# Optimization experiments

Measured on AMD Instinct MI355X. Metric: run time of the kernel, lower is better.

## Reference

```python
import jax, jax.numpy as jnp
import numpy as np

L = 8        # num_layers
B = 4        # batch
S = 1024     # seq_len
D = 1024     # hidden_size
H = 16       # num_heads
FC = 4096    # fc_size
NEG = -1e9   # additive causal-mask value (matches torch code's -1000000000.0)


def setup_inputs() -> dict:
    key = jax.random.key(0)
    ks = jax.random.split(key, 12)
    std = 0.02
    inputs = jax.random.normal(ks[0], (B, S, D), jnp.float32)
    # per-layer stacked parameters; torch Linear y = x W^T + b, here stored as [in, out]
    Wq = jax.random.normal(ks[1], (L, D, D), jnp.float32) * std
    Wk = jax.random.normal(ks[2], (L, D, D), jnp.float32) * std
    Wv = jax.random.normal(ks[3], (L, D, D), jnp.float32) * std
    Wo = jax.random.normal(ks[4], (L, D, D), jnp.float32) * std
    W1 = jax.random.normal(ks[5], (L, D, FC), jnp.float32) * std
    W2 = jax.random.normal(ks[6], (L, FC, D), jnp.float32) * std
    bq = jnp.zeros((L, D), jnp.float32)
    bk = jnp.zeros((L, D), jnp.float32)
    bv = jnp.zeros((L, D), jnp.float32)
    bo = jnp.zeros((L, D), jnp.float32)
    b1 = jnp.zeros((L, FC), jnp.float32)
    b2 = jnp.zeros((L, D), jnp.float32)
    ln_g = jnp.ones((D,), jnp.float32)   # single LayerNorm shared across all sites
    ln_b = jnp.zeros((D,), jnp.float32)
    scale = jnp.asarray(0.1, jnp.float32)  # re-zero residual scale (init 0 in torch; 0.1 for non-degenerate test)
    return dict(inputs=inputs, Wq=Wq, bq=bq, Wk=Wk, bk=bk, Wv=Wv, bv=bv,
                Wo=Wo, bo=bo, W1=W1, b1=b1, W2=W2, b2=b2,
                ln_g=ln_g, ln_b=ln_b, scale=scale)


def reference(inputs, Wq, bq, Wk, bk, Wv, bv, Wo, bo, W1, b1, W2, b2, ln_g, ln_b, scale):
    Bz, Sl, Dm = inputs.shape
    nL = Wq.shape[0]
    dh = Dm // H
    inv_sqrt_dh = 1.0 / np.sqrt(dh).astype(np.float32)

    def layer_norm(x):  # shared gamma/beta, eps matches torch default 1e-5
        mu = jnp.mean(x, axis=-1, keepdims=True)
        var = jnp.var(x, axis=-1, keepdims=True)
        return (x - mu) * jax.lax.rsqrt(var + 1e-5) * ln_g + ln_b

    # causal additive bias [S, S], broadcasts over [B, H, S, S]
    bias = jnp.triu(jnp.full((Sl, Sl), NEG, inputs.dtype), k=1)

    x = inputs
    for i in range(nL):
        # --- masked self-attention block ---
        r = layer_norm(x)
        q = (r @ Wq[i] + bq[i]).reshape(Bz, Sl, H, dh)
        k = (r @ Wk[i] + bk[i]).reshape(Bz, Sl, H, dh)
        v = (r @ Wv[i] + bv[i]).reshape(Bz, Sl, H, dh)
        logits = jnp.einsum('bqhd,bkhd->bhqk', q, k) * inv_sqrt_dh + bias
        attn = jax.nn.softmax(logits, axis=-1)
        vals = jnp.einsum('bhqk,bkhd->bqhd', attn, v).reshape(Bz, Sl, Dm)
        r = vals @ Wo[i] + bo[i]
        x = x + scale * r  # re-zero residual (dropout is identity at inference)
        # --- FFN block ---
        r = layer_norm(x)
        r = jax.nn.gelu(r @ W1[i] + b1[i], approximate=False) @ W2[i] + b2[i]
        x = x + scale * r
    return layer_norm(x)
```

## Files before the change

kernel.cpp:

```cpp
#include <hip/hip_runtime.h>


typedef __bf16 bf16x8 __attribute__((ext_vector_type(8)));
typedef float  f32x4  __attribute__((ext_vector_type(4)));
typedef unsigned int u32x4 __attribute__((ext_vector_type(4)));

#define DEV static __device__ __forceinline__

DEV unsigned short f2bf(float x) {
  unsigned u = __builtin_bit_cast(unsigned int, x);
  u += 0x7fffu + ((u >> 16) & 1u);
  return (unsigned short)(u >> 16);
}

DEV unsigned int pack2bf(float lo, float hi) {
  return (unsigned int)f2bf(lo) | ((unsigned int)f2bf(hi) << 16);
}

DEV f32x4 mfma16(bf16x8 a, bf16x8 b, f32x4 c) {
  return __builtin_amdgcn_mfma_f32_16x16x32_bf16(a, b, c, 0, 0, 0);
}

DEV bf16x8 ldb8(const unsigned short* p) {
  return *reinterpret_cast<const bf16x8*>(p);
}

DEV void gload_lds16(const unsigned short* g, unsigned short* l) {
  __builtin_amdgcn_global_load_lds(
      (const __attribute__((address_space(1))) void*)g,
      (__attribute__((address_space(3))) void*)l, 16, 0, 0);
}

__global__ void transpose_cvt(const float* __restrict__ src,
                              unsigned short* __restrict__ dst,
                              int srcStride, int dstStride) {
  __shared__ float tile[32][33];
  const int t  = threadIdx.x;
  const int r  = t >> 3;
  const int c4 = (t & 7) << 2;
  const int k  = blockIdx.x * 32 + r;
  const int n0 = blockIdx.y * 32 + c4;
  const float4 v = *reinterpret_cast<const float4*>(src + (size_t)k * srcStride + n0);
  tile[r][c4] = v.x; tile[r][c4 + 1] = v.y; tile[r][c4 + 2] = v.z; tile[r][c4 + 3] = v.w;
  __syncthreads();
  const int n  = blockIdx.y * 32 + r;
  const int k0 = blockIdx.x * 32 + c4;
  ushort4 o;
  o.x = f2bf(tile[c4][r]);     o.y = f2bf(tile[c4 + 1][r]);
  o.z = f2bf(tile[c4 + 2][r]); o.w = f2bf(tile[c4 + 3][r]);
  *reinterpret_cast<ushort4*>(dst + (size_t)n * dstStride + k0) = o;
}

__global__ void transpose_cvt4(const float* __restrict__ Wq, const float* __restrict__ Wk,
                               const float* __restrict__ Wv, const float* __restrict__ Wo,
                               unsigned short* __restrict__ Wqkv_t,
                               unsigned short* __restrict__ Wo_t) {
  __shared__ float tile[32][33];
  const int z = blockIdx.z;
  const float* src = (z == 0) ? Wq : (z == 1) ? Wk : (z == 2) ? Wv : Wo;
  unsigned short* dst = (z == 3) ? Wo_t : (Wqkv_t + (size_t)z * 1024 * 1024);
  const int t  = threadIdx.x;
  const int r  = t >> 3;
  const int c4 = (t & 7) << 2;
  const int k  = blockIdx.x * 32 + r;
  const int n0 = blockIdx.y * 32 + c4;
  const float4 v = *reinterpret_cast<const float4*>(src + (size_t)k * 1024 + n0);
  tile[r][c4] = v.x; tile[r][c4 + 1] = v.y; tile[r][c4 + 2] = v.z; tile[r][c4 + 3] = v.w;
  __syncthreads();
  const int n  = blockIdx.y * 32 + r;
  const int k0 = blockIdx.x * 32 + c4;
  ushort4 o;
  o.x = f2bf(tile[c4][r]);     o.y = f2bf(tile[c4 + 1][r]);
  o.z = f2bf(tile[c4 + 2][r]); o.w = f2bf(tile[c4 + 3][r]);
  *reinterpret_cast<ushort4*>(dst + (size_t)n * 1024 + k0) = o;
}

__global__ void pack_qkv_bias(const float* __restrict__ bq, const float* __restrict__ bk,
                              const float* __restrict__ bv, float* __restrict__ out) {
  int i = blockIdx.x * 256 + threadIdx.x;
  out[i] = (i < 1024) ? bq[i] : (i < 2048 ? bk[i - 1024] : bv[i - 2048]);
}

template <int OUTF32>
__global__ __launch_bounds__(256) void ln_kernel(
    const float* x, const float* __restrict__ gam,
    const float* __restrict__ bet, void* out) {
  const int t = threadIdx.x, wave = t >> 6, lane = t & 63;
  const int row = blockIdx.x * 4 + wave;
  const float* xr = x + (size_t)row * 1024;
  float4 v[4];
  float s = 0.f, ss = 0.f;
  #pragma unroll
  for (int k = 0; k < 4; ++k) {
    v[k] = *reinterpret_cast<const float4*>(xr + k * 256 + lane * 4);
    s  += v[k].x + v[k].y + v[k].z + v[k].w;
    ss += v[k].x * v[k].x + v[k].y * v[k].y + v[k].z * v[k].z + v[k].w * v[k].w;
  }
  #pragma unroll
  for (int m = 1; m <= 32; m <<= 1) { s += __shfl_xor(s, m); ss += __shfl_xor(ss, m); }
  const float mean = s * (1.0f / 1024.0f);
  const float var  = ss * (1.0f / 1024.0f) - mean * mean;
  const float rstd = rsqrtf(var + 1e-5f);
  #pragma unroll
  for (int k = 0; k < 4; ++k) {
    const float4 g  = *reinterpret_cast<const float4*>(gam + k * 256 + lane * 4);
    const float4 bb = *reinterpret_cast<const float4*>(bet + k * 256 + lane * 4);
    const float y0 = (v[k].x - mean) * rstd * g.x + bb.x;
    const float y1 = (v[k].y - mean) * rstd * g.y + bb.y;
    const float y2 = (v[k].z - mean) * rstd * g.z + bb.z;
    const float y3 = (v[k].w - mean) * rstd * g.w + bb.w;
    if (OUTF32) {
      float4 o; o.x = y0; o.y = y1; o.z = y2; o.w = y3;
      *reinterpret_cast<float4*>((float*)out + (size_t)row * 1024 + k * 256 + lane * 4) = o;
    } else {
      ushort4 o; o.x = f2bf(y0); o.y = f2bf(y1); o.z = f2bf(y2); o.w = f2bf(y3);
      *reinterpret_cast<ushort4*>((unsigned short*)out + (size_t)row * 1024 + k * 256 + lane * 4) = o;
    }
  }
}

template <int MODE>
__global__ __launch_bounds__(512) void gemm8r(
    const unsigned short* __restrict__ A, const unsigned short* __restrict__ Bt,
    const float* __restrict__ bias, unsigned short* __restrict__ outb,
    unsigned short* __restrict__ vT, int N, int K) {
  __shared__ __attribute__((aligned(16))) unsigned short lds[7 * 8192];
  const int t = threadIdx.x, wave = t >> 6, lane = t & 63;
  const int wm = wave >> 2, wn = wave & 3;
  const int rl15 = lane & 15;

  const int nbn = N >> 8;
  const int qq  = gridDim.x >> 3;
  const int swz = (blockIdx.x & 7) * qq + (blockIdx.x >> 3);
  const int m0 = (swz / nbn) << 8, n0 = (swz % nbn) << 8;

  const unsigned short* aG = A  + (size_t)m0 * K;
  const unsigned short* bG = Bt + (size_t)n0 * K;

  const int srow = lane >> 2;
  const int ssl  = (((lane & 3) ^ ((srow >> 1) & 3)) << 3);
  const int swA  = (((lane >> 4) ^ ((lane >> 1) & 3)) << 3);

  auto stageA = [&](int slot, int kt) {
    #pragma unroll
    for (int j = 0; j < 2; ++j) {
      const int c = wave + j * 8;
      gload_lds16(aG + (size_t)(c * 16 + srow) * K + kt * 32 + ssl,
                  &lds[slot * 8192 + c * 512]);
    }
  };
  auto stageB = [&](int slot, int kt) {
    #pragma unroll
    for (int j = 0; j < 2; ++j) {
      const int c = wave + j * 8;
      gload_lds16(bG + (size_t)(c * 16 + srow) * K + kt * 32 + ssl,
                  &lds[slot * 8192 + c * 512]);
    }
  };

  const int nk = K >> 5;
  stageA(0, 0); stageB(1, 0);
  stageA(2, 1); stageB(3, 1);
  asm volatile("s_waitcnt vmcnt(4)" ::: "memory");
  asm volatile("s_barrier" ::: "memory");

  f32x4 acc[8][4] = {};
  int sA = 0, sB = 1, pA = 4, pB = 5;

  for (int kt = 0; kt < nk; ++kt) {
    const bool more = (kt + 2 < nk);
    if (more) { stageA(pA, kt + 2); stageB(pB, kt + 2); }
    const int ab = sA * 8192, bb = sB * 8192;
    bf16x8 af[8], bfr[4];
    #pragma unroll
    for (int mi = 0; mi < 8; ++mi)
      af[mi] = ldb8(&lds[ab + (wm * 128 + mi * 16 + rl15) * 32 + swA]);
    #pragma unroll
    for (int ni = 0; ni < 4; ++ni)
      bfr[ni] = ldb8(&lds[bb + (wn * 64 + ni * 16 + rl15) * 32 + swA]);
    __builtin_amdgcn_s_setprio(1);
    #pragma unroll
    for (int mi = 0; mi < 8; ++mi)
      #pragma unroll
      for (int ni = 0; ni < 4; ++ni)
        acc[mi][ni] = mfma16(af[mi], bfr[ni], acc[mi][ni]);
    __builtin_amdgcn_s_setprio(0);
    if (more) asm volatile("s_waitcnt vmcnt(4)" ::: "memory");
    else      asm volatile("s_waitcnt vmcnt(0)" ::: "memory");
    asm volatile("s_barrier" ::: "memory");
    sA += 2; if (sA >= 7) sA -= 7;
    sB += 2; if (sB >= 7) sB -= 7;
    pA += 2; if (pA >= 7) pA -= 7;
    pB += 2; if (pB >= 7) pB -= 7;
  }

  const int mrow = m0 + wm * 128 + (lane >> 4) * 4;
  const int ncol = n0 + wn * 64 + rl15;
  #pragma unroll
  for (int ni = 0; ni < 4; ++ni) {
    const int n = ncol + ni * 16;
    const float bn = bias[n];
    #pragma unroll
    for (int mi = 0; mi < 8; ++mi) {
      const int row0 = mrow + mi * 16;
      if constexpr (MODE == 3) {
        if (n >= 2048) {
          const int h = (n - 2048) >> 6, d = (n - 2048) & 63;
          const int b = row0 >> 10, s = row0 & 1023;
          ushort4 o;
          o.x = f2bf(acc[mi][ni][0] + bn); o.y = f2bf(acc[mi][ni][1] + bn);
          o.z = f2bf(acc[mi][ni][2] + bn); o.w = f2bf(acc[mi][ni][3] + bn);
          *reinterpret_cast<ushort4*>(vT + ((size_t)(b * 16 + h) * 64 + d) * 1024 + s) = o;
          continue;
        }
      }
      #pragma unroll
      for (int r = 0; r < 4; ++r) {
        const size_t idx = (size_t)(row0 + r) * N + n;
        float v = acc[mi][ni][r] + bn;
        if constexpr (MODE == 1)
          v = 0.5f * v * (1.0f + erff(v * 0.70710678118f));
        outb[idx] = f2bf(v);
      }
    }
  }
}

template <int MODE, int BN>
__global__ __launch_bounds__(256) void gemm2(
    const unsigned short* __restrict__ A, const unsigned short* __restrict__ Bt,
    const float* __restrict__ bias, unsigned short* __restrict__ outb,
    const float* xin, float* xout, const float* __restrict__ scale_p,
    int N, int K) {
  constexpr int NI = BN / 32;
  constexpr int BSH = BN * 64;
  __shared__ __attribute__((aligned(16))) unsigned short lds[2][8192 + BSH];
  const int t = threadIdx.x, wave = t >> 6, lane = t & 63;
  const int m0 = blockIdx.x * 128, n0 = blockIdx.y * BN;
  const int wm = wave >> 1, wn = wave & 1;

  int srowA[4], scolA[4];
  #pragma unroll
  for (int j = 0; j < 4; ++j) {
    const int c = j * 256 + wave * 64 + lane;
    const int r = c >> 3;
    srowA[j] = r;
    scolA[j] = ((c & 7) ^ (r & 7)) << 3;
  }
  const unsigned short* aBase = A + (size_t)m0 * K;
  const unsigned short* bBase = Bt + (size_t)n0 * K;

  const int xk0 = (((lane >> 4)    ) ^ (lane & 7)) << 3;
  const int xk1 = (((lane >> 4) | 4) ^ (lane & 7)) << 3;
  const int arow = (wm * 64 + (lane & 15)) * 64;
  const int brow = (wn * (BN / 2) + (lane & 15)) * 64;

  f32x4 acc[4][NI] = {};
  const int nk = K >> 6;
  constexpr int BJ = NI;

  {
    unsigned short* l = &lds[0][0];
    #pragma unroll
    for (int j = 0; j < 4; ++j)
      gload_lds16(aBase + (size_t)srowA[j] * K + scolA[j], l + j * 2048 + wave * 512);
    #pragma unroll
    for (int j = 0; j < BJ; ++j)
      gload_lds16(bBase + (size_t)srowA[j] * K + scolA[j], l + 8192 + j * 2048 + wave * 512);
  }
  __syncthreads();

  int cur = 0;
  for (int kt = 0; kt < nk; ++kt) {
    if (kt + 1 < nk) {
      unsigned short* l = &lds[cur ^ 1][0];
      const int ko = (kt + 1) * 64;
      #pragma unroll
      for (int j = 0; j < 4; ++j)
        gload_lds16(aBase + (size_t)srowA[j] * K + ko + scolA[j], l + j * 2048 + wave * 512);
      #pragma unroll
      for (int j = 0; j < BJ; ++j)
        gload_lds16(bBase + (size_t)srowA[j] * K + ko + scolA[j], l + 8192 + j * 2048 + wave * 512);
    }
    const unsigned short* l = &lds[cur][0];
    #pragma unroll
    for (int kc = 0; kc < 2; ++kc) {
      const int xk = kc ? xk1 : xk0;
      bf16x8 a[4], b[NI];
      #pragma unroll
      for (int mi = 0; mi < 4; ++mi) a[mi] = ldb8(&l[arow + mi * 1024 + xk]);
      #pragma unroll
      for (int ni = 0; ni < NI; ++ni) b[ni] = ldb8(&l[8192 + brow + ni * 1024 + xk]);
      __builtin_amdgcn_s_setprio(1);
      #pragma unroll
      for (int mi = 0; mi < 4; ++mi)
        #pragma unroll
        for (int ni = 0; ni < NI; ++ni)
          acc[mi][ni] = mfma16(a[mi], b[ni], acc[mi][ni]);
      __builtin_amdgcn_s_setprio(0);
    }
    __syncthreads();
    cur ^= 1;
  }

  const int mrow = m0 + wm * 64 + (lane >> 4) * 4;
  const int ncol = n0 + wn * (BN / 2) + (lane & 15);
  float scl = 0.f;
  if constexpr (MODE == 2) scl = scale_p[0];
  #pragma unroll
  for (int ni = 0; ni < NI; ++ni) {
    const int n = ncol + ni * 16;
    const float bn = bias[n];
    #pragma unroll
    for (int mi = 0; mi < 4; ++mi) {
      #pragma unroll
      for (int r = 0; r < 4; ++r) {
        const size_t idx = (size_t)(mrow + mi * 16 + r) * N + n;
        float v = acc[mi][ni][r] + bn;
        if constexpr (MODE == 1) {
          v = 0.5f * v * (1.0f + erff(v * 0.70710678118f));
          outb[idx] = f2bf(v);
        } else if constexpr (MODE == 2) {
          xout[idx] = xin[idx] + scl * v;
        } else {
          outb[idx] = f2bf(v);
        }
      }
    }
  }
}

__global__ __launch_bounds__(256) void attn_kernel(
    const unsigned short* __restrict__ qkv, const unsigned short* __restrict__ vT,
    unsigned short* __restrict__ vals) {
  const int bh = blockIdx.x & 63;
  const int g  = 15 - (blockIdx.x >> 6);
  const int b = bh >> 4, h = bh & 15;
  const int t = threadIdx.x, wave = t >> 6, lane = t & 63;
  const int rowLane = lane & 15, grp = lane >> 4;
  const int qt = g * 4 + wave;
  const int q0 = qt * 16;
  const int nkt = (qt >> 2) + 1;

  const unsigned short* qkvB  = qkv + (size_t)b * 1024 * 3072;
  const unsigned short* kBase = qkvB + 1024 + h * 64 + grp * 8;
  const unsigned short* vHead = vT + (size_t)bh * 64 * 1024;

  const unsigned short* qb = qkvB + (size_t)(q0 + rowLane) * 3072 + h * 64 + grp * 8;
  const bf16x8 aq0 = ldb8(qb);
  const bf16x8 aq1 = ldb8(qb + 32);

  f32x4 oaccT[4] = {};
  float mrun = -1e30f, lrun = 0.f;

  bf16x8 k0[4], k1[4];
  #pragma unroll
  for (int nf = 0; nf < 4; ++nf) {
    const unsigned short* kb = kBase + (size_t)(nf * 16 + rowLane) * 3072;
    k0[nf] = ldb8(kb); k1[nf] = ldb8(kb + 32);
  }

  const int srcA = rowLane + ((grp & 1) << 5);
  const int srcB = srcA + 16;
  const bool hiG = (grp >= 2);

  for (int kt = 0; kt < nkt; ++kt) {
    const int kv0 = kt * 64;
    bf16x8 v0[4], v1[4];
    #pragma unroll
    for (int df = 0; df < 4; ++df) {
      const unsigned short* vb = vHead + (size_t)(df * 16 + rowLane) * 1024 + kv0 + grp * 8;
      v0[df] = ldb8(vb); v1[df] = ldb8(vb + 32);
    }
    f32x4 sacc[4];
    #pragma unroll
    for (int nf = 0; nf < 4; ++nf) {
      f32x4 z = {0.f, 0.f, 0.f, 0.f};
      z = mfma16(k0[nf], aq0, z);
      z = mfma16(k1[nf], aq1, z);
      sacc[nf] = z;
    }
    if (kt + 1 < nkt) {
      #pragma unroll
      for (int nf = 0; nf < 4; ++nf) {
        const unsigned short* kb = kBase + (size_t)(kv0 + 64 + nf * 16 + rowLane) * 3072;
        k0[nf] = ldb8(kb); k1[nf] = ldb8(kb + 32);
      }
    }
    float pl[4][4];
    #pragma unroll
    for (int nf = 0; nf < 4; ++nf)
      #pragma unroll
      for (int r = 0; r < 4; ++r) pl[nf][r] = sacc[nf][r] * 0.125f;
    if (kt == nkt - 1) {
      const int qg = q0 + rowLane;
      #pragma unroll
      for (int nf = 0; nf < 4; ++nf)
        #pragma unroll
        for (int r = 0; r < 4; ++r)
          if (kv0 + nf * 16 + grp * 4 + r > qg) pl[nf][r] = -1e30f;
    }
    float mloc = pl[0][0];
    #pragma unroll
    for (int nf = 0; nf < 4; ++nf)
      #pragma unroll
      for (int r = 0; r < 4; ++r) mloc = fmaxf(mloc, pl[nf][r]);
    mloc = fmaxf(mloc, __shfl_xor(mloc, 16));
    mloc = fmaxf(mloc, __shfl_xor(mloc, 32));
    const float mnew = fmaxf(mrun, mloc);
    const float facq = __expf(mrun - mnew);
    mrun = mnew;
    float sloc = 0.f;
    #pragma unroll
    for (int nf = 0; nf < 4; ++nf)
      #pragma unroll
      for (int r = 0; r < 4; ++r) {
        const float e = __expf(pl[nf][r] - mnew);
        pl[nf][r] = e;
        sloc += e;
      }
    sloc += __shfl_xor(sloc, 16);
    sloc += __shfl_xor(sloc, 32);
    lrun = lrun * facq + sloc;
    #pragma unroll
    for (int df = 0; df < 4; ++df)
      #pragma unroll
      for (int r = 0; r < 4; ++r) oaccT[df][r] *= facq;
    unsigned int w0[4], w1[4];
    #pragma unroll
    for (int nf = 0; nf < 4; ++nf) {
      w0[nf] = pack2bf(pl[nf][0], pl[nf][1]);
      w1[nf] = pack2bf(pl[nf][2], pl[nf][3]);
    }
    unsigned int a0, a1, a2, a3, b0, b1, b2, b3;
    {
      const int tA00 = __shfl((int)w0[0], srcA), tA01 = __shfl((int)w0[1], srcA);
      const int tA10 = __shfl((int)w1[0], srcA), tA11 = __shfl((int)w1[1], srcA);
      const int tB00 = __shfl((int)w0[0], srcB), tB01 = __shfl((int)w0[1], srcB);
      const int tB10 = __shfl((int)w1[0], srcB), tB11 = __shfl((int)w1[1], srcB);
      a0 = (unsigned)(hiG ? tA01 : tA00);
      a1 = (unsigned)(hiG ? tA11 : tA10);
      a2 = (unsigned)(hiG ? tB01 : tB00);
      a3 = (unsigned)(hiG ? tB11 : tB10);
      const int uA00 = __shfl((int)w0[2], srcA), uA01 = __shfl((int)w0[3], srcA);
      const int uA10 = __shfl((int)w1[2], srcA), uA11 = __shfl((int)w1[3], srcA);
      const int uB00 = __shfl((int)w0[2], srcB), uB01 = __shfl((int)w0[3], srcB);
      const int uB10 = __shfl((int)w1[2], srcB), uB11 = __shfl((int)w1[3], srcB);
      b0 = (unsigned)(hiG ? uA01 : uA00);
      b1 = (unsigned)(hiG ? uA11 : uA10);
      b2 = (unsigned)(hiG ? uB01 : uB00);
      b3 = (unsigned)(hiG ? uB11 : uB10);
    }
    u32x4 pa0u = {a0, a1, a2, a3};
    u32x4 pa1u = {b0, b1, b2, b3};
    const bf16x8 pa0 = __builtin_bit_cast(bf16x8, pa0u);
    const bf16x8 pa1 = __builtin_bit_cast(bf16x8, pa1u);
    #pragma unroll
    for (int df = 0; df < 4; ++df) {
      oaccT[df] = mfma16(v0[df], pa0, oaccT[df]);
      oaccT[df] = mfma16(v1[df], pa1, oaccT[df]);
    }
  }
  const float rlq = 1.0f / lrun;
  const size_t qrow = (size_t)(b * 1024 + q0 + rowLane) * 1024 + h * 64;
  #pragma unroll
  for (int df = 0; df < 4; ++df) {
    ushort4 o;
    o.x = f2bf(oaccT[df][0] * rlq);
    o.y = f2bf(oaccT[df][1] * rlq);
    o.z = f2bf(oaccT[df][2] * rlq);
    o.w = f2bf(oaccT[df][3] * rlq);
    *reinterpret_cast<ushort4*>(vals + qrow + df * 16 + grp * 4) = o;
  }
}

extern "C" void kernel_launch(void* const* d_in, const int* in_sizes, int n_in,
                              void* d_out, int out_size, void* d_ws, size_t ws_size,
                              hipStream_t stream) {
  (void)in_sizes; (void)n_in; (void)out_size; (void)ws_size;
  const float* inputs = (const float*)d_in[0];
  const float* Wq = (const float*)d_in[1];  const float* bq = (const float*)d_in[2];
  const float* Wk = (const float*)d_in[3];  const float* bk = (const float*)d_in[4];
  const float* Wv = (const float*)d_in[5];  const float* bv = (const float*)d_in[6];
  const float* Wo = (const float*)d_in[7];  const float* bo = (const float*)d_in[8];
  const float* W1 = (const float*)d_in[9];  const float* b1 = (const float*)d_in[10];
  const float* W2 = (const float*)d_in[11]; const float* b2 = (const float*)d_in[12];
  const float* ln_g = (const float*)d_in[13];
  const float* ln_b = (const float*)d_in[14];
  const float* scale_p = (const float*)d_in[15];
  float* xbuf = (float*)d_out;

  char* w = (char*)d_ws;
  size_t off = 0;
  auto take = [&](size_t bytes) {
    void* p = w + off;
    off = (off + bytes + 255) & ~(size_t)255;
    return p;
  };
  unsigned short* Wqkv_t = (unsigned short*)take((size_t)3072 * 1024 * 2);
  unsigned short* Wo_t   = (unsigned short*)take((size_t)1024 * 1024 * 2);
  unsigned short* W1_t   = (unsigned short*)take((size_t)4096 * 1024 * 2);
  unsigned short* W2_t   = (unsigned short*)take((size_t)1024 * 4096 * 2);
  float*          bqkv   = (float*)take(3072 * 4);
  unsigned short* rbuf   = (unsigned short*)take((size_t)4096 * 1024 * 2);
  unsigned short* qkvb   = (unsigned short*)take((size_t)4096 * 3072 * 2);
  unsigned short* vTb    = (unsigned short*)take((size_t)64 * 64 * 1024 * 2);
  unsigned short* valsb  = (unsigned short*)take((size_t)4096 * 1024 * 2);
  unsigned short* hbuf   = (unsigned short*)take((size_t)4096 * 4096 * 2);

  for (int i = 0; i < 8; ++i) {
    const float* xin = (i == 0) ? inputs : xbuf;
    transpose_cvt4<<<dim3(32, 32, 4), 256, 0, stream>>>(
        Wq + (size_t)i * 1024 * 1024, Wk + (size_t)i * 1024 * 1024,
        Wv + (size_t)i * 1024 * 1024, Wo + (size_t)i * 1024 * 1024, Wqkv_t, Wo_t);
    transpose_cvt<<<dim3(32, 128), 256, 0, stream>>>(W1 + (size_t)i * 1024 * 4096, W1_t, 4096, 1024);
    transpose_cvt<<<dim3(128, 32), 256, 0, stream>>>(W2 + (size_t)i * 4096 * 1024, W2_t, 1024, 4096);
    pack_qkv_bias<<<12, 256, 0, stream>>>(bq + i * 1024, bk + i * 1024, bv + i * 1024, bqkv);
    ln_kernel<0><<<1024, 256, 0, stream>>>(xin, ln_g, ln_b, rbuf);
    gemm8r<3><<<192, 512, 0, stream>>>(rbuf, Wqkv_t, bqkv, qkvb, vTb, 3072, 1024);
    attn_kernel<<<1024, 256, 0, stream>>>(qkvb, vTb, valsb);
    gemm2<2, 64><<<dim3(32, 16), 256, 0, stream>>>(valsb, Wo_t, bo + i * 1024, nullptr,
                                                   xin, xbuf, scale_p, 1024, 1024);
    ln_kernel<0><<<1024, 256, 0, stream>>>(xbuf, ln_g, ln_b, rbuf);
    gemm8r<1><<<256, 512, 0, stream>>>(rbuf, W1_t, b1 + i * 4096, hbuf, nullptr, 4096, 1024);
    gemm2<2, 64><<<dim3(32, 16), 256, 0, stream>>>(hbuf, W2_t, b2 + i * 1024, nullptr,
                                                   xbuf, xbuf, scale_p, 1024, 4096);
  }
  ln_kernel<1><<<1024, 256, 0, stream>>>(xbuf, ln_g, ln_b, xbuf);
}
```

Baseline: 2.083 ms.

## Split attention KV range across wave pairs and balance causal q-tiles

Each attention block now handles two query tiles paired as p and 63-p, so every block does roughly equal causal work. For each query tile, two waves split the KV tiles in half, and the grid doubles to 2048 blocks. The partial outputs and their max/sum statistics are merged through shared memory with a log-sum-exp rescale before the bf16 store. This aims to cut load imbalance and the serial KV loop length, at the cost of a shared-memory merge, one block barrier and half the waves idling during the final write.

```diff
diff --git a/kernel.cpp b/kernel.cpp
--- a/kernel.cpp
+++ b/kernel.cpp
@@ -334,13 +334,22 @@
     const unsigned short* __restrict__ qkv, const unsigned short* __restrict__ vT,
     unsigned short* __restrict__ vals) {
   const int bh = blockIdx.x & 63;
-  const int g  = 15 - (blockIdx.x >> 6);
+  const int p  = blockIdx.x >> 6;
   const int b = bh >> 4, h = bh & 15;
   const int t = threadIdx.x, wave = t >> 6, lane = t & 63;
   const int rowLane = lane & 15, grp = lane >> 4;
-  const int qt = g * 4 + wave;
-  const int q0 = qt * 16;
+
+  const int s01 = ((wave >> 1) ^ (p & 1)) & 1;
+  const int u   = wave & 1;
+  const int qt  = s01 ? (63 - p) : p;
+  const int q0  = qt * 16;
   const int nkt = (qt >> 2) + 1;
+  const int hlf = (nkt + 1) >> 1;
+  const int kt0   = u ? hlf : 0;
+  const int ktEnd = u ? nkt : hlf;
+
+  __shared__ float Om[2][16][68];
+  __shared__ float Ml[2][16][2];
 
   const unsigned short* qkvB  = qkv + (size_t)b * 1024 * 3072;
   const unsigned short* kBase = qkvB + 1024 + h * 64 + grp * 8;
@@ -354,17 +363,19 @@
   float mrun = -1e30f, lrun = 0.f;
 
   bf16x8 k0[4], k1[4];
-  #pragma unroll
-  for (int nf = 0; nf < 4; ++nf) {
-    const unsigned short* kb = kBase + (size_t)(nf * 16 + rowLane) * 3072;
-    k0[nf] = ldb8(kb); k1[nf] = ldb8(kb + 32);
+  if (kt0 < ktEnd) {
+    #pragma unroll
+    for (int nf = 0; nf < 4; ++nf) {
+      const unsigned short* kb = kBase + (size_t)(kt0 * 64 + nf * 16 + rowLane) * 3072;
+      k0[nf] = ldb8(kb); k1[nf] = ldb8(kb + 32);
+    }
   }
 
   const int srcA = rowLane + ((grp & 1) << 5);
   const int srcB = srcA + 16;
   const bool hiG = (grp >= 2);
 
-  for (int kt = 0; kt < nkt; ++kt) {
+  for (int kt = kt0; kt < ktEnd; ++kt) {
     const int kv0 = kt * 64;
     bf16x8 v0[4], v1[4];
     #pragma unroll
@@ -380,7 +391,7 @@
       z = mfma16(k1[nf], aq1, z);
       sacc[nf] = z;
     }
-    if (kt + 1 < nkt) {
+    if (kt + 1 < ktEnd) {
       #pragma unroll
       for (int nf = 0; nf < 4; ++nf) {
         const unsigned short* kb = kBase + (size_t)(kv0 + 64 + nf * 16 + rowLane) * 3072;
@@ -461,16 +472,36 @@
       oaccT[df] = mfma16(v1[df], pa1, oaccT[df]);
     }
   }
-  const float rlq = 1.0f / lrun;
-  const size_t qrow = (size_t)(b * 1024 + q0 + rowLane) * 1024 + h * 64;
-  #pragma unroll
-  for (int df = 0; df < 4; ++df) {
-    ushort4 o;
-    o.x = f2bf(oaccT[df][0] * rlq);
-    o.y = f2bf(oaccT[df][1] * rlq);
-    o.z = f2bf(oaccT[df][2] * rlq);
-    o.w = f2bf(oaccT[df][3] * rlq);
-    *reinterpret_cast<ushort4*>(vals + qrow + df * 16 + grp * 4) = o;
+
+  if (u) {
+    #pragma unroll
+    for (int df = 0; df < 4; ++df) {
+      float4 o; o.x = oaccT[df][0]; o.y = oaccT[df][1];
+      o.z = oaccT[df][2]; o.w = oaccT[df][3];
+      *reinterpret_cast<float4*>(&Om[s01][rowLane][df * 16 + grp * 4]) = o;
+    }
+    if (grp == 0) { Ml[s01][rowLane][0] = mrun; Ml[s01][rowLane][1] = lrun; }
+  }
+  __syncthreads();
+  if (!u) {
+    const float m1 = Ml[s01][rowLane][0];
+    const float l1 = Ml[s01][rowLane][1];
+    const float mm = fmaxf(mrun, m1);
+    const float e0 = __expf(mrun - mm);
+    const float e1 = __expf(m1 - mm);
+    const float rl = 1.0f / (lrun * e0 + l1 * e1);
+    const size_t qrow = (size_t)(b * 1024 + q0 + rowLane) * 1024 + h * 64;
+    #pragma unroll
+    for (int df = 0; df < 4; ++df) {
+      ushort4 o;
+      #pragma unroll
+      for (int r = 0; r < 4; ++r) {
+        const float ov = (oaccT[df][r] * e0 +
+                          Om[s01][rowLane][df * 16 + grp * 4 + r] * e1) * rl;
+        ((unsigned short*)&o)[r] = f2bf(ov);
+      }
+      *reinterpret_cast<ushort4*>(vals + qrow + df * 16 + grp * 4) = o;
+    }
   }
 }
 
@@ -518,7 +549,7 @@
     pack_qkv_bias<<<12, 256, 0, stream>>>(bq + i * 1024, bk + i * 1024, bv + i * 1024, bqkv);
     ln_kernel<0><<<1024, 256, 0, stream>>>(xin, ln_g, ln_b, rbuf);
     gemm8r<3><<<192, 512, 0, stream>>>(rbuf, Wqkv_t, bqkv, qkvb, vTb, 3072, 1024);
-    attn_kernel<<<1024, 256, 0, stream>>>(qkvb, vTb, valsb);
+    attn_kernel<<<2048, 256, 0, stream>>>(qkvb, vTb, valsb);
     gemm2<2, 64><<<dim3(32, 16), 256, 0, stream>>>(valsb, Wo_t, bo + i * 1024, nullptr,
                                                    xin, xbuf, scale_p, 1024, 1024);
     ln_kernel<0><<<1024, 256, 0, stream>>>(xbuf, ln_g, ln_b, rbuf);
```

Result: no change. 2.100 ms (+0.8%).
